# Kernel tuning notes

Measured on AMD Instinct MI355X. Metric: run time of the kernel, lower is better.

The kernel has to match this reference:

```python
import jax, jax.numpy as jnp
import numpy as np

N_NODES = 100000
N_EDGES = 3200000


def gcn_conv(x, W, b, src, dst, n_nodes):
    """PyG GCNConv: self-loops, symmetric D^-1/2 A D^-1/2 norm, linear, bias."""
    loop = jnp.arange(n_nodes, dtype=src.dtype)
    s = jnp.concatenate([src, loop])  # [E+N]
    d = jnp.concatenate([dst, loop])  # [E+N]
    # degree computed at destination (col), edge_weight = 1
    deg = jax.ops.segment_sum(jnp.ones_like(d, dtype=x.dtype), d,
                              num_segments=n_nodes)
    dinv = jnp.where(deg > 0, jax.lax.rsqrt(deg), 0.0)
    norm = dinv[s] * dinv[d]  # [E+N]
    h = x @ W.T  # [N, out]
    msg = h[s] * norm[:, None]  # gather + scale, [E+N, out]
    out = jax.ops.segment_sum(msg, d, num_segments=n_nodes)  # scatter-add
    return out + b


def setup_inputs() -> dict:
    key = jax.random.key(0)
    k1, k2, k3, k4 = jax.random.split(key, 4)
    x = jax.random.normal(k1, (N_NODES, 2), dtype=jnp.float32)
    edge_index = jax.random.randint(k2, (2, N_EDGES), 0, N_NODES,
                                    dtype=jnp.int64)
    # Glorot-ish init for linear weights
    W1 = jax.random.normal(k3, (64, 2), dtype=jnp.float32) * 0.5
    b1 = jnp.zeros((64,), dtype=jnp.float32)
    W2 = jax.random.normal(k4, (2, 64), dtype=jnp.float32) * 0.125
    b2 = jnp.zeros((2,), dtype=jnp.float32)
    return {"x": x, "edge_index": edge_index, "W1": W1, "b1": b1,
            "W2": W2, "b2": b2}


def reference(x, edge_index, W1, b1, W2, b2):
    src, dst = edge_index[0], edge_index[1]
    h = gcn_conv(x, W1, b1, src, dst, N_NODES)
    h = jax.nn.relu(h)
    out = gcn_conv(h, W2, b2, src, dst, N_NODES)
    return out
```

## Files before the change

### kernel.cpp

```cpp
#include <hip/hip_runtime.h>

#define N_NODES 100000
#define SHIFT 8
#define BNODES 256
#define NB 391
#define CAP 9728
#define TILE 8192
#define SB 1024


__global__ __launch_bounds__(SB, 8) void k_sort(const int* __restrict__ src,
                                                const int* __restrict__ dst,
                                                int* claim, int* sg, int e) {
    __shared__ int hist[2 * NB];
    __shared__ int rank[2 * NB];
    __shared__ int addrbase[NB];
    __shared__ int partials[16];
    __shared__ int stage[TILE];
    __shared__ unsigned short binmap[TILE];

    const int t = threadIdx.x;
    const int base = blockIdx.x * TILE;
    const int n = min(TILE, e - base);
    const int goff = (t >> 9) * NB;

    for (int i = t; i < 2 * NB; i += SB) hist[i] = 0;
    __syncthreads();

    int recs[8];
    int bins[8];
    int* myh = hist + goff;
#pragma unroll
    for (int k = 0; k < 2; ++k) {
        int idx = base + (k * SB + t) * 4;
        if (idx + 3 < e) {
            int4 s4 = *(const int4*)(src + idx);
            int4 d4 = *(const int4*)(dst + idx);
            int ss[4] = {s4.x, s4.y, s4.z, s4.w};
            int dd[4] = {d4.x, d4.y, d4.z, d4.w};
#pragma unroll
            for (int j = 0; j < 4; ++j) {
                int b = dd[j] >> SHIFT;
                bins[4 * k + j] = b;
                recs[4 * k + j] = ss[j] | ((dd[j] & (BNODES - 1)) << 17);
                atomicAdd(&myh[b], 1);
            }
        } else {
#pragma unroll
            for (int j = 0; j < 4; ++j) {
                int i2 = idx + j;
                if (i2 < e) {
                    int d = dst[i2];
                    int b = d >> SHIFT;
                    bins[4 * k + j] = b;
                    recs[4 * k + j] = src[i2] | ((d & (BNODES - 1)) << 17);
                    atomicAdd(&myh[b], 1);
                } else {
                    bins[4 * k + j] = -1;
                }
            }
        }
    }
    __syncthreads();

    int c0 = 0, c1 = 0, c = 0;
    if (t < NB) {
        c0 = hist[t];
        c1 = hist[NB + t];
        c = c0 + c1;
    }
    int vs = c;
#pragma unroll
    for (int off = 1; off < 64; off <<= 1) {
        int w = __shfl_up(vs, off, 64);
        if ((t & 63) >= off) vs += w;
    }
    if ((t & 63) == 63) partials[t >> 6] = vs;
    __syncthreads();
    int add = 0;
    for (int w = 0; w < (t >> 6); ++w) add += partials[w];
    vs += add;
    int excl = vs - c;
    if (t < NB) {
        rank[t] = excl;
        rank[NB + t] = excl + c0;
        int rb = c ? atomicAdd(&claim[t], c) : 0;
        addrbase[t] = t * CAP + rb - excl;
    }
    __syncthreads();

    int* myr = rank + goff;
#pragma unroll
    for (int m = 0; m < 8; ++m) {
        int b = bins[m];
        if (b >= 0) {
            int pos = atomicAdd(&myr[b], 1);
            stage[pos] = recs[m];
            binmap[pos] = (unsigned short)b;
        }
    }
    __syncthreads();

    for (int i = t; i < n; i += SB) {
        sg[addrbase[binmap[i]] + i] = stage[i];
    }
}

__global__ __launch_bounds__(1024) void k_refine(const int* __restrict__ claim,
                                                 const int* __restrict__ sg,
                                                 const float* __restrict__ x,
                                                 int* sg2, int* packed,
                                                 float2* u) {
    __shared__ int hist[4 * BNODES];
    __shared__ int rank[4 * BNODES];
    __shared__ int partials[4];
    const int t = threadIdx.x;
    const int b = blockIdx.x;
    const int* p = sg + b * CAP;
    const int len = claim[b];
    const int g = t >> 8;

    int4 r[3];
#pragma unroll
    for (int k = 0; k < 3; ++k) {
        int idx = 4 * t + 4096 * k;
        int4 v = make_int4(-1, -1, -1, -1);
        if (idx + 3 < len) v = *(const int4*)(p + idx);
        else if (idx < len) {
            v.x = p[idx];
            if (idx + 1 < len) v.y = p[idx + 1];
            if (idx + 2 < len) v.z = p[idx + 2];
        }
        r[k] = v;
    }
    for (int i = t; i < 4 * BNODES; i += 1024) hist[i] = 0;
    __syncthreads();
    int* myh = hist + g * BNODES;
#pragma unroll
    for (int k = 0; k < 3; ++k) {
        if (r[k].x != -1) atomicAdd(&myh[((unsigned)r[k].x) >> 17], 1);
        if (r[k].y != -1) atomicAdd(&myh[((unsigned)r[k].y) >> 17], 1);
        if (r[k].z != -1) atomicAdd(&myh[((unsigned)r[k].z) >> 17], 1);
        if (r[k].w != -1) atomicAdd(&myh[((unsigned)r[k].w) >> 17], 1);
    }
    __syncthreads();

    int c4x = 0, c4y = 0, c4z = 0, c4w = 0, tot = 0;
    if (t < BNODES) {
        c4x = hist[t];
        c4y = hist[BNODES + t];
        c4z = hist[2 * BNODES + t];
        c4w = hist[3 * BNODES + t];
        tot = (c4x + c4y) + (c4z + c4w);
    }
    int vs = tot;
#pragma unroll
    for (int off = 1; off < 64; off <<= 1) {
        int w = __shfl_up(vs, off, 64);
        if ((t & 63) >= off) vs += w;
    }
    if ((t & 63) == 63 && t < BNODES) partials[t >> 6] = vs;
    __syncthreads();
    if (t < BNODES) {
        int add = 0;
        for (int w = 0; w < (t >> 6); ++w) add += partials[w];
        vs += add;
        int excl = vs - tot;
        int run = excl;
        rank[t] = run; run += c4x;
        rank[BNODES + t] = run; run += c4y;
        rank[2 * BNODES + t] = run; run += c4z;
        rank[3 * BNODES + t] = run;
        int node = b * BNODES + t;
        if (node < N_NODES) {
            packed[node] = (b * CAP + excl) | (tot << 22);
            float dv = rsqrtf((float)(tot + 1));
            float2 xv = ((const float2*)x)[node];
            u[node] = make_float2(dv * xv.x, dv * xv.y);
        }
    }
    __syncthreads();

    int* q = sg2 + b * CAP;
    int* myr = rank + g * BNODES;
#pragma unroll
    for (int k = 0; k < 3; ++k) {
        if (r[k].x != -1) q[atomicAdd(&myr[((unsigned)r[k].x) >> 17], 1)] = r[k].x & 0x1FFFF;
        if (r[k].y != -1) q[atomicAdd(&myr[((unsigned)r[k].y) >> 17], 1)] = r[k].y & 0x1FFFF;
        if (r[k].z != -1) q[atomicAdd(&myr[((unsigned)r[k].z) >> 17], 1)] = r[k].z & 0x1FFFF;
        if (r[k].w != -1) q[atomicAdd(&myr[((unsigned)r[k].w) >> 17], 1)] = r[k].w & 0x1FFFF;
    }
}

__global__ __launch_bounds__(256) void k_agg1(const int* __restrict__ sg2,
                                              const int* __restrict__ packed,
                                              const float2* __restrict__ u,
                                              const float* __restrict__ W1,
                                              const float* __restrict__ b1,
                                              const float* __restrict__ W2,
                                              float2* v) {
    __shared__ float sW1[128], sb1[64], sW2[128];
    int t = threadIdx.x;
    if (t < 128) { sW1[t] = W1[t]; sW2[t] = W2[t]; }
    else if (t < 192) sb1[t - 128] = b1[t - 128];
    __syncthreads();
    int n = blockIdx.x * 32 + (t >> 3);
    if (n >= N_NODES) return;
    int g = t & 7;
    int pk = packed[n];
    int s = pk & 0x3FFFFF;
    int cnt = ((unsigned)pk) >> 22;
    int e2 = s + cnt;
    float sx = 0.f, sy = 0.f;
    int i = s + g;
    for (; i + 24 < e2; i += 32) {
        float2 ga = u[sg2[i]];
        float2 gb = u[sg2[i + 8]];
        float2 gc = u[sg2[i + 16]];
        float2 gd = u[sg2[i + 24]];
        sx += (ga.x + gb.x) + (gc.x + gd.x);
        sy += (ga.y + gb.y) + (gc.y + gd.y);
    }
    for (; i + 8 < e2; i += 16) {
        float2 ga = u[sg2[i]];
        float2 gb = u[sg2[i + 8]];
        sx += ga.x + gb.x;
        sy += ga.y + gb.y;
    }
    if (i < e2) { float2 ga = u[sg2[i]]; sx += ga.x; sy += ga.y; }
    sx += __shfl_xor(sx, 1, 8); sy += __shfl_xor(sy, 1, 8);
    sx += __shfl_xor(sx, 2, 8); sy += __shfl_xor(sy, 2, 8);
    sx += __shfl_xor(sx, 4, 8); sy += __shfl_xor(sy, 4, 8);
    float dv = rsqrtf((float)(cnt + 1));
    float2 un = u[n];
    float a0 = dv * (sx + un.x), a1 = dv * (sy + un.y);
    float y0 = 0.f, y1 = 0.f;
#pragma unroll
    for (int k = 0; k < 8; ++k) {
        int j = g + 8 * k;
        float h = fmaxf(fmaf(sW1[2 * j], a0,
                        fmaf(sW1[2 * j + 1], a1, sb1[j])), 0.f);
        y0 = fmaf(sW2[j], h, y0);
        y1 = fmaf(sW2[64 + j], h, y1);
    }
    y0 += __shfl_xor(y0, 1, 8); y1 += __shfl_xor(y1, 1, 8);
    y0 += __shfl_xor(y0, 2, 8); y1 += __shfl_xor(y1, 2, 8);
    y0 += __shfl_xor(y0, 4, 8); y1 += __shfl_xor(y1, 4, 8);
    if (g == 0) v[n] = make_float2(dv * y0, dv * y1);
}

__global__ __launch_bounds__(256) void k_agg2(const int* __restrict__ sg2,
                                              const int* __restrict__ packed,
                                              const float2* __restrict__ v,
                                              const float* __restrict__ b2,
                                              float2* out) {
    int t = threadIdx.x;
    int n = blockIdx.x * 32 + (t >> 3);
    if (n >= N_NODES) return;
    int g = t & 7;
    int pk = packed[n];
    int s = pk & 0x3FFFFF;
    int cnt = ((unsigned)pk) >> 22;
    int e2 = s + cnt;
    float sx = 0.f, sy = 0.f;
    int i = s + g;
    for (; i + 24 < e2; i += 32) {
        float2 ga = v[sg2[i]];
        float2 gb = v[sg2[i + 8]];
        float2 gc = v[sg2[i + 16]];
        float2 gd = v[sg2[i + 24]];
        sx += (ga.x + gb.x) + (gc.x + gd.x);
        sy += (ga.y + gb.y) + (gc.y + gd.y);
    }
    for (; i + 8 < e2; i += 16) {
        float2 ga = v[sg2[i]];
        float2 gb = v[sg2[i + 8]];
        sx += ga.x + gb.x;
        sy += ga.y + gb.y;
    }
    if (i < e2) { float2 ga = v[sg2[i]]; sx += ga.x; sy += ga.y; }
    sx += __shfl_xor(sx, 1, 8); sy += __shfl_xor(sy, 1, 8);
    sx += __shfl_xor(sx, 2, 8); sy += __shfl_xor(sy, 2, 8);
    sx += __shfl_xor(sx, 4, 8); sy += __shfl_xor(sy, 4, 8);
    if (g == 0) {
        float dv = rsqrtf((float)(cnt + 1));
        float2 vn = v[n];
        out[n] = make_float2(fmaf(dv, sx + vn.x, b2[0]),
                             fmaf(dv, sy + vn.y, b2[1]));
    }
}

extern "C" void kernel_launch(void* const* d_in, const int* in_sizes, int n_in,
                              void* d_out, int out_size, void* d_ws, size_t ws_size,
                              hipStream_t stream) {
    const float* x  = (const float*)d_in[0];
    const int* ei   = (const int*)d_in[1];
    const float* W1 = (const float*)d_in[2];
    const float* b1 = (const float*)d_in[3];
    const float* W2 = (const float*)d_in[4];
    const float* b2 = (const float*)d_in[5];

    int e = in_sizes[1] / 2;
    const int* src = ei;
    const int* dst = ei + e;

    int* ws      = (int*)d_ws;
    int* claim   = ws;
    int* sg      = ws + ((NB + 3) & ~3);
    int* sg2     = sg + NB * CAP;
    int* packed  = sg2 + NB * CAP;
    float2* u    = (float2*)(packed + N_NODES);
    float2* v    = u + N_NODES;
    float2* outp = (float2*)d_out;

    hipMemsetAsync(claim, 0, NB * sizeof(int), stream);

    const int gA = (N_NODES + 31) / 32;
    k_sort  <<<(e + TILE - 1) / TILE, SB, 0, stream>>>(src, dst, claim, sg, e);
    k_refine<<<NB, 1024, 0, stream>>>(claim, sg, x, sg2, packed, u);
    k_agg1  <<<gA, 256, 0, stream>>>(sg2, packed, u, W1, b1, W2, v);
    k_agg2  <<<gA, 256, 0, stream>>>(sg2, packed, v, b2, outp);
}
```

Before: 149.1 us.

## Merge per-node offset/count and scaled features into one float4; use 16 lanes per node

```diff
diff --git a/kernel.cpp b/kernel.cpp
--- a/kernel.cpp
+++ b/kernel.cpp
@@ -109,8 +109,7 @@
 __global__ __launch_bounds__(1024) void k_refine(const int* __restrict__ claim,
                                                  const int* __restrict__ sg,
                                                  const float* __restrict__ x,
-                                                 int* sg2, int* packed,
-                                                 float2* u) {
+                                                 int* sg2, float4* meta) {
     __shared__ int hist[4 * BNODES];
     __shared__ int rank[4 * BNODES];
     __shared__ int partials[4];
@@ -173,10 +172,11 @@
         rank[3 * BNODES + t] = run;
         int node = b * BNODES + t;
         if (node < N_NODES) {
-            packed[node] = (b * CAP + excl) | (tot << 22);
             float dv = rsqrtf((float)(tot + 1));
             float2 xv = ((const float2*)x)[node];
-            u[node] = make_float2(dv * xv.x, dv * xv.y);
+            meta[node] = make_float4(dv * xv.x, dv * xv.y,
+                                     __int_as_float(b * CAP + excl),
+                                     __int_as_float(tot));
         }
     }
     __syncthreads();
@@ -193,8 +193,7 @@
 }
 
 __global__ __launch_bounds__(256) void k_agg1(const int* __restrict__ sg2,
-                                              const int* __restrict__ packed,
-                                              const float2* __restrict__ u,
+                                              const float4* __restrict__ meta,
                                               const float* __restrict__ W1,
                                               const float* __restrict__ b1,
                                               const float* __restrict__ W2,
@@ -204,84 +203,70 @@
     if (t < 128) { sW1[t] = W1[t]; sW2[t] = W2[t]; }
     else if (t < 192) sb1[t - 128] = b1[t - 128];
     __syncthreads();
-    int n = blockIdx.x * 32 + (t >> 3);
+    int n = blockIdx.x * 16 + (t >> 4);
     if (n >= N_NODES) return;
-    int g = t & 7;
-    int pk = packed[n];
-    int s = pk & 0x3FFFFF;
-    int cnt = ((unsigned)pk) >> 22;
+    int g = t & 15;
+    float4 mt = meta[n];
+    int s = __float_as_int(mt.z);
+    int cnt = __float_as_int(mt.w);
     int e2 = s + cnt;
     float sx = 0.f, sy = 0.f;
     int i = s + g;
-    for (; i + 24 < e2; i += 32) {
-        float2 ga = u[sg2[i]];
-        float2 gb = u[sg2[i + 8]];
-        float2 gc = u[sg2[i + 16]];
-        float2 gd = u[sg2[i + 24]];
-        sx += (ga.x + gb.x) + (gc.x + gd.x);
-        sy += (ga.y + gb.y) + (gc.y + gd.y);
-    }
-    for (; i + 8 < e2; i += 16) {
-        float2 ga = u[sg2[i]];
-        float2 gb = u[sg2[i + 8]];
+    for (; i + 16 < e2; i += 32) {
+        float4 ga = meta[sg2[i]];
+        float4 gb = meta[sg2[i + 16]];
         sx += ga.x + gb.x;
         sy += ga.y + gb.y;
     }
-    if (i < e2) { float2 ga = u[sg2[i]]; sx += ga.x; sy += ga.y; }
-    sx += __shfl_xor(sx, 1, 8); sy += __shfl_xor(sy, 1, 8);
-    sx += __shfl_xor(sx, 2, 8); sy += __shfl_xor(sy, 2, 8);
-    sx += __shfl_xor(sx, 4, 8); sy += __shfl_xor(sy, 4, 8);
+    if (i < e2) { float4 ga = meta[sg2[i]]; sx += ga.x; sy += ga.y; }
+    sx += __shfl_xor(sx, 1, 16); sy += __shfl_xor(sy, 1, 16);
+    sx += __shfl_xor(sx, 2, 16); sy += __shfl_xor(sy, 2, 16);
+    sx += __shfl_xor(sx, 4, 16); sy += __shfl_xor(sy, 4, 16);
+    sx += __shfl_xor(sx, 8, 16); sy += __shfl_xor(sy, 8, 16);
     float dv = rsqrtf((float)(cnt + 1));
-    float2 un = u[n];
-    float a0 = dv * (sx + un.x), a1 = dv * (sy + un.y);
+    float a0 = dv * (sx + mt.x), a1 = dv * (sy + mt.y);
     float y0 = 0.f, y1 = 0.f;
 #pragma unroll
-    for (int k = 0; k < 8; ++k) {
-        int j = g + 8 * k;
+    for (int k = 0; k < 4; ++k) {
+        int j = g + 16 * k;
         float h = fmaxf(fmaf(sW1[2 * j], a0,
                         fmaf(sW1[2 * j + 1], a1, sb1[j])), 0.f);
         y0 = fmaf(sW2[j], h, y0);
         y1 = fmaf(sW2[64 + j], h, y1);
     }
-    y0 += __shfl_xor(y0, 1, 8); y1 += __shfl_xor(y1, 1, 8);
-    y0 += __shfl_xor(y0, 2, 8); y1 += __shfl_xor(y1, 2, 8);
-    y0 += __shfl_xor(y0, 4, 8); y1 += __shfl_xor(y1, 4, 8);
+    y0 += __shfl_xor(y0, 1, 16); y1 += __shfl_xor(y1, 1, 16);
+    y0 += __shfl_xor(y0, 2, 16); y1 += __shfl_xor(y1, 2, 16);
+    y0 += __shfl_xor(y0, 4, 16); y1 += __shfl_xor(y1, 4, 16);
+    y0 += __shfl_xor(y0, 8, 16); y1 += __shfl_xor(y1, 8, 16);
     if (g == 0) v[n] = make_float2(dv * y0, dv * y1);
 }
 
 __global__ __launch_bounds__(256) void k_agg2(const int* __restrict__ sg2,
-                                              const int* __restrict__ packed,
+                                              const float4* __restrict__ meta,
                                               const float2* __restrict__ v,
                                               const float* __restrict__ b2,
                                               float2* out) {
     int t = threadIdx.x;
-    int n = blockIdx.x * 32 + (t >> 3);
+    int n = blockIdx.x * 16 + (t >> 4);
     if (n >= N_NODES) return;
-    int g = t & 7;
-    int pk = packed[n];
-    int s = pk & 0x3FFFFF;
-    int cnt = ((unsigned)pk) >> 22;
+    int g = t & 15;
+    float4 mt = meta[n];
+    int s = __float_as_int(mt.z);
+    int cnt = __float_as_int(mt.w);
     int e2 = s + cnt;
     float sx = 0.f, sy = 0.f;
     int i = s + g;
-    for (; i + 24 < e2; i += 32) {
+    for (; i + 16 < e2; i += 32) {
         float2 ga = v[sg2[i]];
-        float2 gb = v[sg2[i + 8]];
-        float2 gc = v[sg2[i + 16]];
-        float2 gd = v[sg2[i + 24]];
-        sx += (ga.x + gb.x) + (gc.x + gd.x);
-        sy += (ga.y + gb.y) + (gc.y + gd.y);
-    }
-    for (; i + 8 < e2; i += 16) {
-        float2 ga = v[sg2[i]];
-        float2 gb = v[sg2[i + 8]];
+        float2 gb = v[sg2[i + 16]];
         sx += ga.x + gb.x;
         sy += ga.y + gb.y;
     }
     if (i < e2) { float2 ga = v[sg2[i]]; sx += ga.x; sy += ga.y; }
-    sx += __shfl_xor(sx, 1, 8); sy += __shfl_xor(sy, 1, 8);
-    sx += __shfl_xor(sx, 2, 8); sy += __shfl_xor(sy, 2, 8);
-    sx += __shfl_xor(sx, 4, 8); sy += __shfl_xor(sy, 4, 8);
+    sx += __shfl_xor(sx, 1, 16); sy += __shfl_xor(sy, 1, 16);
+    sx += __shfl_xor(sx, 2, 16); sy += __shfl_xor(sy, 2, 16);
+    sx += __shfl_xor(sx, 4, 16); sy += __shfl_xor(sy, 4, 16);
+    sx += __shfl_xor(sx, 8, 16); sy += __shfl_xor(sy, 8, 16);
     if (g == 0) {
         float dv = rsqrtf((float)(cnt + 1));
         float2 vn = v[n];
@@ -308,16 +293,15 @@
     int* claim   = ws;
     int* sg      = ws + ((NB + 3) & ~3);
     int* sg2     = sg + NB * CAP;
-    int* packed  = sg2 + NB * CAP;
-    float2* u    = (float2*)(packed + N_NODES);
-    float2* v    = u + N_NODES;
+    float4* meta = (float4*)(sg2 + NB * CAP);
+    float2* v    = (float2*)(meta + N_NODES);
     float2* outp = (float2*)d_out;
 
     hipMemsetAsync(claim, 0, NB * sizeof(int), stream);
 
-    const int gA = (N_NODES + 31) / 32;
+    const int gA = (N_NODES + 15) / 16;
     k_sort  <<<(e + TILE - 1) / TILE, SB, 0, stream>>>(src, dst, claim, sg, e);
-    k_refine<<<NB, 1024, 0, stream>>>(claim, sg, x, sg2, packed, u);
-    k_agg1  <<<gA, 256, 0, stream>>>(sg2, packed, u, W1, b1, W2, v);
-    k_agg2  <<<gA, 256, 0, stream>>>(sg2, packed, v, b2, outp);
-}
+    k_refine<<<NB, 1024, 0, stream>>>(claim, sg, x, sg2, meta);
+    k_agg1  <<<gA, 256, 0, stream>>>(sg2, meta, W1, b1, W2, v);
+    k_agg2  <<<gA, 256, 0, stream>>>(sg2, meta, v, b2, outp);
+}
```

Result: slower. 152.3 us (+2.2%).
